# Performance work log

Hardware: AMD Instinct MI355X
Metric: run time of the kernel (lower is better)

## Reference

```python
import jax, jax.numpy as jnp
import numpy as np

FEAT_DIM = 256
NUM_HEADS = 8
HEAD_DIM = FEAT_DIM // NUM_HEADS
N_NODES = 4096
LN_EPS = 1e-5


def setup_inputs() -> dict:
    key = jax.random.key(0)
    ks = jax.random.split(key, 10)
    C = FEAT_DIM
    s = 1.0 / np.sqrt(C)
    x = jax.random.normal(ks[0], (N_NODES, C), dtype=jnp.float32)
    Wq = jax.random.uniform(ks[1], (C, C), jnp.float32, -s, s)
    bq = jax.random.uniform(ks[2], (C,), jnp.float32, -s, s)
    Wk = jax.random.uniform(ks[3], (C, C), jnp.float32, -s, s)
    bk = jax.random.uniform(ks[4], (C,), jnp.float32, -s, s)
    Wv = jax.random.uniform(ks[5], (C, C), jnp.float32, -s, s)
    bv = jax.random.uniform(ks[6], (C,), jnp.float32, -s, s)
    Wo = jax.random.uniform(ks[7], (C, C), jnp.float32, -s, s)
    bo = jax.random.uniform(ks[8], (C,), jnp.float32, -s, s)
    scale = jnp.float32(1.0 / np.sqrt(HEAD_DIM))
    gamma = jnp.ones((C,), jnp.float32)
    beta = jnp.zeros((C,), jnp.float32)
    return {"x": x, "Wq": Wq, "bq": bq, "Wk": Wk, "bk": bk, "Wv": Wv,
            "bv": bv, "scale": scale, "Wo": Wo, "bo": bo,
            "gamma": gamma, "beta": beta}


def reference(x, Wq, bq, Wk, bk, Wv, bv, scale, Wo, bo, gamma, beta):
    N, C = x.shape
    H, D = NUM_HEADS, HEAD_DIM
    q = (x @ Wq + bq).reshape(N, H, D)
    k = (x @ Wk + bk).reshape(N, H, D)
    v = (x @ Wv + bv).reshape(N, H, D)
    # scores[i, j, h]; softmax over j (the key/node axis), per original dim=1
    scores = jnp.einsum('ihd,jhd->ijh', q, k) * scale
    attn = jax.nn.softmax(scores, axis=1)
    messages = jnp.einsum('ijh,jhd->ihd', attn, v).reshape(N, H * D)
    y = x + messages @ Wo + bo
    # LayerNorm over last dim
    mu = jnp.mean(y, axis=-1, keepdims=True)
    var = jnp.mean(jnp.square(y - mu), axis=-1, keepdims=True)
    return (y - mu) * jax.lax.rsqrt(var + LN_EPS) * gamma + beta
```

## Files before the change

### kernel.cpp

```cpp
#include <hip/hip_runtime.h>
#include <hip/hip_bf16.h>
#include <math.h>

#define NN 4096
#define C  256
#define NH 8
#define HD 32
#define LN_EPS 1e-5f
#define LOG2E 1.44269504088896340736f

typedef unsigned short u16;
typedef __attribute__((ext_vector_type(8))) short bf16x8;
typedef __attribute__((ext_vector_type(4))) float f32x4;

__device__ inline u16 f2b(float f) {
    union { float f; unsigned u; } v; v.f = f;
    unsigned r = (v.u + 0x7fff + ((v.u >> 16) & 1)) >> 16;
    return (u16)r;
}

__device__ inline float fexp2(float x) {
#if __has_builtin(__builtin_amdgcn_exp2f)
    return __builtin_amdgcn_exp2f(x);
#else
    return exp2f(x);
#endif
}

__device__ inline unsigned pack_trunc(float e0, float e1) {
    return __builtin_amdgcn_perm(__float_as_uint(e1), __float_as_uint(e0),
                                 0x07060302u);
}

__device__ inline void atomic_add_agent(float* p, float v) {
    __hip_atomic_fetch_add(p, v, __ATOMIC_RELAXED, __HIP_MEMORY_SCOPE_AGENT);
}

__global__ __launch_bounds__(256) void prep_kernel(
    const float* __restrict__ Wq, const float* __restrict__ Wk,
    const float* __restrict__ Wv, const float* __restrict__ Wo,
    const float* __restrict__ x,
    u16* __restrict__ WqkvT, u16* __restrict__ WoT, u16* __restrict__ xb)
{
    const int z = blockIdx.z;
    if (z < 4) {
        __shared__ float tile[32][33];
        const float* W = (z == 0) ? Wq : (z == 1) ? Wk : (z == 2) ? Wv : Wo;
        u16* WT = (z == 3) ? WoT : (WqkvT + (size_t)z * 256 * 256);
        const int tx = threadIdx.x & 31, ty = threadIdx.x >> 5;
        const int n0 = blockIdx.x * 32, k0 = blockIdx.y * 32;
        #pragma unroll
        for (int i = 0; i < 32; i += 8)
            tile[ty + i][tx] = W[(size_t)(k0 + ty + i) * 256 + n0 + tx];
        __syncthreads();
        #pragma unroll
        for (int i = 0; i < 32; i += 8)
            WT[(size_t)(n0 + ty + i) * 256 + k0 + tx] = f2b(tile[tx][ty + i]);
    } else {
        const int slice = z - 4;
        const int bid = blockIdx.x * 8 + blockIdx.y;
        const int base = slice * (NN * C / 4) + bid * 4096 + threadIdx.x * 16;
        #pragma unroll
        for (int i = 0; i < 4; ++i) {
            const float4 v = *(const float4*)(x + base + i * 4);
            union { u16 u[4]; unsigned long long ull; } pk;
            pk.u[0] = f2b(v.x); pk.u[1] = f2b(v.y);
            pk.u[2] = f2b(v.z); pk.u[3] = f2b(v.w);
            *(unsigned long long*)(xb + base + i * 4) = pk.ull;
        }
    }
}

#define TRS 80
__global__ __launch_bounds__(256) void qkv_mfma_kernel(
    const u16* __restrict__ xb, const u16* __restrict__ WT,
    const float* __restrict__ bq, const float* __restrict__ bk,
    const float* __restrict__ bv, const float* __restrict__ scale_p,
    u16* __restrict__ qb, u16* __restrict__ kb, u16* __restrict__ vT)
{
    __shared__ u16 tr[64 * TRS];
    const int m0 = blockIdx.x * 64;
    const int n0 = blockIdx.y * 64;
    const int t = threadIdx.x;
    const int wave = t >> 6, lane = t & 63;
    const int l16 = lane & 15, quad = lane >> 4;

    f32x4 acc[4];
    #pragma unroll
    for (int ct = 0; ct < 4; ++ct) acc[ct] = f32x4{0.f, 0.f, 0.f, 0.f};

    const u16* xrow = xb + (size_t)(m0 + wave * 16 + l16) * C;
    #pragma unroll
    for (int kk = 0; kk < 8; ++kk) {
        const bf16x8 af = *(const bf16x8*)(xrow + kk * 32 + quad * 8);
        #pragma unroll
        for (int ct = 0; ct < 4; ++ct) {
            const bf16x8 bfr = *(const bf16x8*)(
                WT + (size_t)(n0 + ct * 16 + l16) * C + kk * 32 + quad * 8);
            acc[ct] = __builtin_amdgcn_mfma_f32_16x16x32_bf16(af, bfr, acc[ct], 0, 0, 0);
        }
    }

    const int sect = n0 >> 8;
    const int c0 = n0 & 255;
    const int rloc = wave * 16 + quad * 4;
    if (sect == 2) {
        #pragma unroll
        for (int ct = 0; ct < 4; ++ct) {
            const int c = c0 + ct * 16 + l16;
            const float b = bv[c];
            union { u16 u[4]; unsigned long long ull; } pk;
            #pragma unroll
            for (int r = 0; r < 4; ++r) pk.u[r] = f2b(acc[ct][r] + b);
            *(unsigned long long*)(vT + (size_t)c * NN + m0 + rloc) = pk.ull;
        }
    } else {
        const float scl = (sect == 0) ? (*scale_p) * LOG2E : 1.f;
        const float* bias = (sect == 0) ? bq : bk;
        #pragma unroll
        for (int ct = 0; ct < 4; ++ct) {
            const float b = bias[c0 + ct * 16 + l16];
            #pragma unroll
            for (int r = 0; r < 4; ++r)
                tr[(rloc + r) * TRS + ct * 16 + l16] = f2b((acc[ct][r] + b) * scl);
        }
        __syncthreads();
        const int row = t >> 2, chunk = t & 3;
        u16* dst = ((sect == 0) ? qb : kb)
                   + (size_t)(m0 + row) * C + c0 + chunk * 16;
        const u16* src = tr + row * TRS + chunk * 16;
        *(bf16x8*)(dst)     = *(const bf16x8*)(src);
        *(bf16x8*)(dst + 8) = *(const bf16x8*)(src + 8);
    }
}

#define TQ 64
#define TJ 64
#define NZ 4
#define ZT (NN / NZ)
#define KSTRIDE 40
#define VSTRIDE 72

__global__ __launch_bounds__(256) void attn_mfma_kernel(
    const u16* __restrict__ q, const u16* __restrict__ k,
    const u16* __restrict__ vT, float* __restrict__ msgacc,
    float* __restrict__ lacc)
{
    __shared__ u16 Ks[TJ * KSTRIDE];
    __shared__ u16 Vs[HD * VSTRIDE];
    __shared__ u16 Ps[4][16 * VSTRIDE];

    const int qbase = blockIdx.x * TQ;
    const int h = blockIdx.y;
    const int z = blockIdx.z;
    const int t = threadIdx.x;
    const int wave = t >> 6;
    const int lane = t & 63;
    const int l16 = lane & 15;
    const int quad = lane >> 4;

    const bf16x8 qfrag = *(const bf16x8*)(
        q + (size_t)(qbase + wave * 16 + l16) * C + h * HD + quad * 8);

    float lsum = 0.f;
    f32x4 o0 = {0.f, 0.f, 0.f, 0.f};
    f32x4 o1 = {0.f, 0.f, 0.f, 0.f};

    const int sj = t >> 2, sc = t & 3;
    const int sd = t >> 3, se = t & 7;

    for (int j0 = z * ZT; j0 < z * ZT + ZT; j0 += TJ) {
        __syncthreads();
        *(bf16x8*)(Ks + sj * KSTRIDE + sc * 8) =
            *(const bf16x8*)(k + (size_t)(j0 + sj) * C + h * HD + sc * 8);
        *(bf16x8*)(Vs + sd * VSTRIDE + se * 8) =
            *(const bf16x8*)(vT + (size_t)(h * HD + sd) * NN + j0 + se * 8);
        __syncthreads();

        f32x4 st[4];
        #pragma unroll
        for (int ct = 0; ct < 4; ++ct) {
            const bf16x8 kf = *(const bf16x8*)(Ks + (ct * 16 + l16) * KSTRIDE + quad * 8);
            f32x4 zz = {0.f, 0.f, 0.f, 0.f};
            st[ct] = __builtin_amdgcn_mfma_f32_16x16x32_bf16(kf, qfrag, zz, 0, 0, 0);
        }

        #pragma unroll
        for (int ct = 0; ct < 4; ++ct) {
            const float e0 = fexp2(st[ct][0]);
            const float e1 = fexp2(st[ct][1]);
            const float e2 = fexp2(st[ct][2]);
            const float e3 = fexp2(st[ct][3]);
            lsum += (e0 + e1) + (e2 + e3);
            const unsigned lo = pack_trunc(e0, e1);
            const unsigned hi = pack_trunc(e2, e3);
            *(unsigned long long*)(&Ps[wave][l16 * VSTRIDE + ct * 16 + quad * 4]) =
                (unsigned long long)lo | ((unsigned long long)hi << 32);
        }

        asm volatile("s_waitcnt lgkmcnt(0)" ::: "memory");

        #pragma unroll
        for (int ks = 0; ks < 2; ++ks) {
            const bf16x8 pf = *(const bf16x8*)(&Ps[wave][l16 * VSTRIDE + ks * 32 + quad * 8]);
            const bf16x8 vf0 = *(const bf16x8*)(Vs + l16 * VSTRIDE + ks * 32 + quad * 8);
            const bf16x8 vf1 = *(const bf16x8*)(Vs + (16 + l16) * VSTRIDE + ks * 32 + quad * 8);
            o0 = __builtin_amdgcn_mfma_f32_16x16x32_bf16(pf, vf0, o0, 0, 0, 0);
            o1 = __builtin_amdgcn_mfma_f32_16x16x32_bf16(pf, vf1, o1, 0, 0, 0);
        }
    }

    lsum += __shfl_xor(lsum, 16);
    lsum += __shfl_xor(lsum, 32);
    if (quad == 0)
        atomic_add_agent(&lacc[(size_t)(qbase + wave * 16 + l16) * NH + h], lsum);

    #pragma unroll
    for (int r = 0; r < 4; ++r) {
        const int row = qbase + wave * 16 + quad * 4 + r;
        atomic_add_agent(&msgacc[(size_t)row * C + h * HD + l16], o0[r]);
        atomic_add_agent(&msgacc[(size_t)row * C + h * HD + 16 + l16], o1[r]);
    }
}

#define OROWS 8
__global__ __launch_bounds__(256) void out_ln_mfma_kernel(
    const float* __restrict__ msgacc, const float* __restrict__ lacc,
    const u16* __restrict__ WoT, const float* __restrict__ bo,
    const float* __restrict__ x, const float* __restrict__ gamma,
    const float* __restrict__ beta, float* __restrict__ out)
{
    __shared__ float sums[2][4][OROWS];
    const int m0 = blockIdx.x * OROWS;
    const int t = threadIdx.x;
    const int w = t >> 6, lane = t & 63;
    const int l16 = lane & 15, quad = lane >> 4;

    f32x4 acc[4];
    #pragma unroll
    for (int ct = 0; ct < 4; ++ct) acc[ct] = f32x4{0.f, 0.f, 0.f, 0.f};

    const int ar = min(m0 + l16, NN - 1);
    const float* arow = msgacc + (size_t)ar * C;
    const float* lrow = lacc + (size_t)ar * NH;
    #pragma unroll
    for (int kk = 0; kk < 8; ++kk) {
        const float li = 1.f / lrow[kk];
        const float4 a0 = *(const float4*)(arow + kk * 32 + quad * 8);
        const float4 a1 = *(const float4*)(arow + kk * 32 + quad * 8 + 4);
        union { unsigned u[4]; bf16x8 v; } af;
        af.u[0] = pack_trunc(a0.x * li, a0.y * li);
        af.u[1] = pack_trunc(a0.z * li, a0.w * li);
        af.u[2] = pack_trunc(a1.x * li, a1.y * li);
        af.u[3] = pack_trunc(a1.z * li, a1.w * li);
        #pragma unroll
        for (int ct = 0; ct < 4; ++ct) {
            const bf16x8 bfr = *(const bf16x8*)(
                WoT + (size_t)(w * 64 + ct * 16 + l16) * C + kk * 32 + quad * 8);
            acc[ct] = __builtin_amdgcn_mfma_f32_16x16x32_bf16(af.v, bfr, acc[ct], 0, 0, 0);
        }
    }

    float val[4][4];
    if (quad < 2) {
        #pragma unroll
        for (int r = 0; r < 4; ++r) {
            const int row = m0 + quad * 4 + r;
            float sr = 0.f, qr = 0.f;
            #pragma unroll
            for (int ct = 0; ct < 4; ++ct) {
                const int c = w * 64 + ct * 16 + l16;
                const float v = acc[ct][r] + bo[c] + x[(size_t)row * C + c];
                val[ct][r] = v;
                sr += v;
                qr = fmaf(v, v, qr);
            }
            sr += __shfl_xor(sr, 1); sr += __shfl_xor(sr, 2);
            sr += __shfl_xor(sr, 4); sr += __shfl_xor(sr, 8);
            qr += __shfl_xor(qr, 1); qr += __shfl_xor(qr, 2);
            qr += __shfl_xor(qr, 4); qr += __shfl_xor(qr, 8);
            if (l16 == 0) {
                sums[0][w][quad * 4 + r] = sr;
                sums[1][w][quad * 4 + r] = qr;
            }
        }
    }
    __syncthreads();

    if (quad < 2) {
        #pragma unroll
        for (int r = 0; r < 4; ++r) {
            const int ri = quad * 4 + r;
            const int row = m0 + ri;
            const float tot  = sums[0][0][ri] + sums[0][1][ri] + sums[0][2][ri] + sums[0][3][ri];
            const float tot2 = sums[1][0][ri] + sums[1][1][ri] + sums[1][2][ri] + sums[1][3][ri];
            const float mu = tot * (1.f / C);
            const float var = fmaxf(tot2 * (1.f / C) - mu * mu, 0.f);
            const float rstd = rsqrtf(var + LN_EPS);
            #pragma unroll
            for (int ct = 0; ct < 4; ++ct) {
                const int c = w * 64 + ct * 16 + l16;
                out[(size_t)row * C + c] = (val[ct][r] - mu) * rstd * gamma[c] + beta[c];
            }
        }
    }
}

extern "C" void kernel_launch(void* const* d_in, const int* in_sizes, int n_in,
                              void* d_out, int out_size, void* d_ws, size_t ws_size,
                              hipStream_t stream) {
    const float* x     = (const float*)d_in[0];
    const float* Wq    = (const float*)d_in[1];
    const float* bq    = (const float*)d_in[2];
    const float* Wk    = (const float*)d_in[3];
    const float* bk    = (const float*)d_in[4];
    const float* Wv    = (const float*)d_in[5];
    const float* bv    = (const float*)d_in[6];
    const float* scale = (const float*)d_in[7];
    const float* Wo    = (const float*)d_in[8];
    const float* bo    = (const float*)d_in[9];
    const float* gamma = (const float*)d_in[10];
    const float* beta  = (const float*)d_in[11];
    float* out = (float*)d_out;

    u16* qb     = (u16*)d_ws;
    u16* kb     = qb + (size_t)NN * C;
    u16* vT     = kb + (size_t)NN * C;
    u16* xbuf   = vT + (size_t)NN * C;
    u16* WqkvT  = xbuf + (size_t)NN * C;
    u16* WoT    = WqkvT + (size_t)3 * C * C;
    float* msgacc = (float*)(WoT + (size_t)C * C);
    float* lacc   = msgacc + (size_t)NN * C;

    hipMemsetAsync(msgacc, 0, ((size_t)NN * C + (size_t)NN * NH) * sizeof(float),
                   stream);

    prep_kernel<<<dim3(8, 8, 8), 256, 0, stream>>>(Wq, Wk, Wv, Wo, x,
                                                   WqkvT, WoT, xbuf);
    qkv_mfma_kernel<<<dim3(NN / 64, 12), 256, 0, stream>>>(
        xbuf, WqkvT, bq, bk, bv, scale, qb, kb, vT);
    attn_mfma_kernel<<<dim3(NN / TQ, NH, NZ), 256, 0, stream>>>(
        qb, kb, vT, msgacc, lacc);
    out_ln_mfma_kernel<<<NN / OROWS, 256, 0, stream>>>(msgacc, lacc, WoT, bo, x,
                                                       gamma, beta, out);
}
```

Before: 158.0 us.

## Fuse all stages into one persistent cooperative kernel with grid syncs

```diff
diff --git a/kernel.cpp b/kernel.cpp
--- a/kernel.cpp
+++ b/kernel.cpp
@@ -1,6 +1,9 @@
 #include <hip/hip_runtime.h>
+#include <hip/hip_cooperative_groups.h>
 #include <hip/hip_bf16.h>
 #include <math.h>
+
+namespace cg = cooperative_groups;
 
 #define NN 4096
 #define C  256
@@ -13,6 +16,14 @@
 typedef __attribute__((ext_vector_type(8))) short bf16x8;
 typedef __attribute__((ext_vector_type(4))) float f32x4;
 
+#define TQ 64
+#define TJ 64
+#define KSTRIDE 40
+#define VSTRIDE 72
+#define TRS 80
+#define OROWS 8
+#define ZERO_FLOATS ((size_t)NN * C + (size_t)NN * NH)
+
 __device__ inline u16 f2b(float f) {
     union { float f; unsigned u; } v; v.f = f;
     unsigned r = (v.u + 0x7fff + ((v.u >> 16) & 1)) >> 16;
@@ -36,271 +47,281 @@
     __hip_atomic_fetch_add(p, v, __ATOMIC_RELAXED, __HIP_MEMORY_SCOPE_AGENT);
 }
 
-__global__ __launch_bounds__(256) void prep_kernel(
-    const float* __restrict__ Wq, const float* __restrict__ Wk,
-    const float* __restrict__ Wv, const float* __restrict__ Wo,
+struct SMemAttn {
+    u16 Ks[TJ * KSTRIDE];
+    u16 Vs[HD * VSTRIDE];
+    u16 Ps[4][16 * VSTRIDE];
+};
+union SMem {
+    SMemAttn a;
+    float tile[32][33];
+    u16 tr[64 * TRS];
+    float sums[2][4][OROWS];
+};
+
+__global__ __launch_bounds__(256, 6) void fused_kernel(
     const float* __restrict__ x,
-    u16* __restrict__ WqkvT, u16* __restrict__ WoT, u16* __restrict__ xb)
+    const float* __restrict__ Wq, const float* __restrict__ bq,
+    const float* __restrict__ Wk, const float* __restrict__ bk,
+    const float* __restrict__ Wv, const float* __restrict__ bv,
+    const float* __restrict__ scale_p,
+    const float* __restrict__ Wo, const float* __restrict__ bo,
+    const float* __restrict__ gamma, const float* __restrict__ beta,
+    float* __restrict__ out,
+    u16* __restrict__ qb, u16* __restrict__ kb, u16* __restrict__ vT,
+    u16* __restrict__ xbuf, u16* __restrict__ WqkvT, u16* __restrict__ WoT,
+    float* __restrict__ msgacc, float* __restrict__ lacc, int NZC)
 {
-    const int z = blockIdx.z;
-    if (z < 4) {
-        __shared__ float tile[32][33];
-        const float* W = (z == 0) ? Wq : (z == 1) ? Wk : (z == 2) ? Wv : Wo;
-        u16* WT = (z == 3) ? WoT : (WqkvT + (size_t)z * 256 * 256);
-        const int tx = threadIdx.x & 31, ty = threadIdx.x >> 5;
-        const int n0 = blockIdx.x * 32, k0 = blockIdx.y * 32;
-        #pragma unroll
-        for (int i = 0; i < 32; i += 8)
-            tile[ty + i][tx] = W[(size_t)(k0 + ty + i) * 256 + n0 + tx];
-        __syncthreads();
-        #pragma unroll
-        for (int i = 0; i < 32; i += 8)
-            WT[(size_t)(n0 + ty + i) * 256 + k0 + tx] = f2b(tile[tx][ty + i]);
-    } else {
-        const int slice = z - 4;
-        const int bid = blockIdx.x * 8 + blockIdx.y;
-        const int base = slice * (NN * C / 4) + bid * 4096 + threadIdx.x * 16;
-        #pragma unroll
-        for (int i = 0; i < 4; ++i) {
-            const float4 v = *(const float4*)(x + base + i * 4);
-            union { u16 u[4]; unsigned long long ull; } pk;
-            pk.u[0] = f2b(v.x); pk.u[1] = f2b(v.y);
-            pk.u[2] = f2b(v.z); pk.u[3] = f2b(v.w);
-            *(unsigned long long*)(xb + base + i * 4) = pk.ull;
-        }
-    }
-}
-
-#define TRS 80
-__global__ __launch_bounds__(256) void qkv_mfma_kernel(
-    const u16* __restrict__ xb, const u16* __restrict__ WT,
-    const float* __restrict__ bq, const float* __restrict__ bk,
-    const float* __restrict__ bv, const float* __restrict__ scale_p,
-    u16* __restrict__ qb, u16* __restrict__ kb, u16* __restrict__ vT)
-{
-    __shared__ u16 tr[64 * TRS];
-    const int m0 = blockIdx.x * 64;
-    const int n0 = blockIdx.y * 64;
+    __shared__ SMem sm;
+    cg::grid_group grid = cg::this_grid();
+    const int G = gridDim.x;
     const int t = threadIdx.x;
     const int wave = t >> 6, lane = t & 63;
     const int l16 = lane & 15, quad = lane >> 4;
 
-    f32x4 acc[4];
-    #pragma unroll
-    for (int ct = 0; ct < 4; ++ct) acc[ct] = f32x4{0.f, 0.f, 0.f, 0.f};
-
-    const u16* xrow = xb + (size_t)(m0 + wave * 16 + l16) * C;
-    #pragma unroll
-    for (int kk = 0; kk < 8; ++kk) {
-        const bf16x8 af = *(const bf16x8*)(xrow + kk * 32 + quad * 8);
-        #pragma unroll
-        for (int ct = 0; ct < 4; ++ct) {
-            const bf16x8 bfr = *(const bf16x8*)(
-                WT + (size_t)(n0 + ct * 16 + l16) * C + kk * 32 + quad * 8);
-            acc[ct] = __builtin_amdgcn_mfma_f32_16x16x32_bf16(af, bfr, acc[ct], 0, 0, 0);
-        }
-    }
-
-    const int sect = n0 >> 8;
-    const int c0 = n0 & 255;
-    const int rloc = wave * 16 + quad * 4;
-    if (sect == 2) {
-        #pragma unroll
-        for (int ct = 0; ct < 4; ++ct) {
-            const int c = c0 + ct * 16 + l16;
-            const float b = bv[c];
-            union { u16 u[4]; unsigned long long ull; } pk;
-            #pragma unroll
-            for (int r = 0; r < 4; ++r) pk.u[r] = f2b(acc[ct][r] + b);
-            *(unsigned long long*)(vT + (size_t)c * NN + m0 + rloc) = pk.ull;
-        }
-    } else {
-        const float scl = (sect == 0) ? (*scale_p) * LOG2E : 1.f;
-        const float* bias = (sect == 0) ? bq : bk;
-        #pragma unroll
-        for (int ct = 0; ct < 4; ++ct) {
-            const float b = bias[c0 + ct * 16 + l16];
-            #pragma unroll
-            for (int r = 0; r < 4; ++r)
-                tr[(rloc + r) * TRS + ct * 16 + l16] = f2b((acc[ct][r] + b) * scl);
-        }
+    {
+        const size_t start = ((size_t)blockIdx.x * 256 + t) * 4;
+        const size_t step = (size_t)G * 1024;
+        const float4 zf = {0.f, 0.f, 0.f, 0.f};
+        for (size_t i = start; i < ZERO_FLOATS; i += step)
+            *(float4*)(msgacc + i) = zf;
+    }
+    for (int job = blockIdx.x; job < 512; job += G) {
+        if (job < 256) {
+            const int z = job >> 6;
+            const int sub = job & 63;
+            const int n0 = (sub & 7) * 32, k0 = (sub >> 3) * 32;
+            const float* W = (z == 0) ? Wq : (z == 1) ? Wk : (z == 2) ? Wv : Wo;
+            u16* WT = (z == 3) ? WoT : (WqkvT + (size_t)z * 65536);
+            const int tx = t & 31, ty = t >> 5;
+            __syncthreads();
+            #pragma unroll
+            for (int i = 0; i < 32; i += 8)
+                sm.tile[ty + i][tx] = W[(size_t)(k0 + ty + i) * 256 + n0 + tx];
+            __syncthreads();
+            #pragma unroll
+            for (int i = 0; i < 32; i += 8)
+                WT[(size_t)(n0 + ty + i) * 256 + k0 + tx] = f2b(sm.tile[tx][ty + i]);
+        } else {
+            const int base = (job - 256) * 4096 + t * 16;
+            #pragma unroll
+            for (int i = 0; i < 4; ++i) {
+                const float4 v = *(const float4*)(x + base + i * 4);
+                union { u16 u[4]; unsigned long long ull; } pk;
+                pk.u[0] = f2b(v.x); pk.u[1] = f2b(v.y);
+                pk.u[2] = f2b(v.z); pk.u[3] = f2b(v.w);
+                *(unsigned long long*)(xbuf + base + i * 4) = pk.ull;
+            }
+        }
+    }
+    grid.sync();
+
+    for (int job = blockIdx.x; job < 768; job += G) {
+        const int m0 = (job & 63) * 64;
+        const int n0 = (job >> 6) * 64;
+
+        f32x4 acc[4];
+        #pragma unroll
+        for (int ct = 0; ct < 4; ++ct) acc[ct] = f32x4{0.f, 0.f, 0.f, 0.f};
+
+        const u16* xrow = xbuf + (size_t)(m0 + wave * 16 + l16) * C;
+        #pragma unroll
+        for (int kk = 0; kk < 8; ++kk) {
+            const bf16x8 af = *(const bf16x8*)(xrow + kk * 32 + quad * 8);
+            #pragma unroll
+            for (int ct = 0; ct < 4; ++ct) {
+                const bf16x8 bfr = *(const bf16x8*)(
+                    WqkvT + (size_t)(n0 + ct * 16 + l16) * C + kk * 32 + quad * 8);
+                acc[ct] = __builtin_amdgcn_mfma_f32_16x16x32_bf16(af, bfr, acc[ct], 0, 0, 0);
+            }
+        }
+
+        const int sect = n0 >> 8;
+        const int c0 = n0 & 255;
+        const int rloc = wave * 16 + quad * 4;
+        if (sect == 2) {
+            #pragma unroll
+            for (int ct = 0; ct < 4; ++ct) {
+                const int c = c0 + ct * 16 + l16;
+                const float b = bv[c];
+                union { u16 u[4]; unsigned long long ull; } pk;
+                #pragma unroll
+                for (int r = 0; r < 4; ++r) pk.u[r] = f2b(acc[ct][r] + b);
+                *(unsigned long long*)(vT + (size_t)c * NN + m0 + rloc) = pk.ull;
+            }
+        } else {
+            const float scl = (sect == 0) ? (*scale_p) * LOG2E : 1.f;
+            const float* bias = (sect == 0) ? bq : bk;
+            __syncthreads();
+            #pragma unroll
+            for (int ct = 0; ct < 4; ++ct) {
+                const float b = bias[c0 + ct * 16 + l16];
+                #pragma unroll
+                for (int r = 0; r < 4; ++r)
+                    sm.tr[(rloc + r) * TRS + ct * 16 + l16] =
+                        f2b((acc[ct][r] + b) * scl);
+            }
+            __syncthreads();
+            const int row = t >> 2, chunk = t & 3;
+            u16* dst = ((sect == 0) ? qb : kb)
+                       + (size_t)(m0 + row) * C + c0 + chunk * 16;
+            const u16* src = sm.tr + row * TRS + chunk * 16;
+            *(bf16x8*)(dst)     = *(const bf16x8*)(src);
+            *(bf16x8*)(dst + 8) = *(const bf16x8*)(src + 8);
+        }
+    }
+    grid.sync();
+
+    for (int job = blockIdx.x; job < 512 * NZC; job += G) {
+        const int qbase = (job & 63) * TQ;
+        const int h = (job >> 6) & 7;
+        const int z = job >> 9;
+        const int tile0 = (64 * z) / NZC, tile1 = (64 * (z + 1)) / NZC;
+
+        const bf16x8 qfrag = *(const bf16x8*)(
+            qb + (size_t)(qbase + wave * 16 + l16) * C + h * HD + quad * 8);
+
+        float lsum = 0.f;
+        f32x4 o0 = {0.f, 0.f, 0.f, 0.f};
+        f32x4 o1 = {0.f, 0.f, 0.f, 0.f};
+
+        const int sj = t >> 2, sc = t & 3;
+        const int sd = t >> 3, se = t & 7;
+
+        for (int j0 = tile0 * TJ; j0 < tile1 * TJ; j0 += TJ) {
+            __syncthreads();
+            *(bf16x8*)(sm.a.Ks + sj * KSTRIDE + sc * 8) =
+                *(const bf16x8*)(kb + (size_t)(j0 + sj) * C + h * HD + sc * 8);
+            *(bf16x8*)(sm.a.Vs + sd * VSTRIDE + se * 8) =
+                *(const bf16x8*)(vT + (size_t)(h * HD + sd) * NN + j0 + se * 8);
+            __syncthreads();
+
+            f32x4 st[4];
+            #pragma unroll
+            for (int ct = 0; ct < 4; ++ct) {
+                const bf16x8 kf = *(const bf16x8*)(
+                    sm.a.Ks + (ct * 16 + l16) * KSTRIDE + quad * 8);
+                f32x4 zz = {0.f, 0.f, 0.f, 0.f};
+                st[ct] = __builtin_amdgcn_mfma_f32_16x16x32_bf16(kf, qfrag, zz, 0, 0, 0);
+            }
+
+            #pragma unroll
+            for (int ct = 0; ct < 4; ++ct) {
+                const float e0 = fexp2(st[ct][0]);
+                const float e1 = fexp2(st[ct][1]);
+                const float e2 = fexp2(st[ct][2]);
+                const float e3 = fexp2(st[ct][3]);
+                lsum += (e0 + e1) + (e2 + e3);
+                const unsigned lo = pack_trunc(e0, e1);
+                const unsigned hi = pack_trunc(e2, e3);
+                *(unsigned long long*)(
+                    &sm.a.Ps[wave][l16 * VSTRIDE + ct * 16 + quad * 4]) =
+                    (unsigned long long)lo | ((unsigned long long)hi << 32);
+            }
+
+            asm volatile("s_waitcnt lgkmcnt(0)" ::: "memory");
+
+            #pragma unroll
+            for (int ks = 0; ks < 2; ++ks) {
+                const bf16x8 pf = *(const bf16x8*)(
+                    &sm.a.Ps[wave][l16 * VSTRIDE + ks * 32 + quad * 8]);
+                const bf16x8 vf0 = *(const bf16x8*)(
+                    sm.a.Vs + l16 * VSTRIDE + ks * 32 + quad * 8);
+                const bf16x8 vf1 = *(const bf16x8*)(
+                    sm.a.Vs + (16 + l16) * VSTRIDE + ks * 32 + quad * 8);
+                o0 = __builtin_amdgcn_mfma_f32_16x16x32_bf16(pf, vf0, o0, 0, 0, 0);
+                o1 = __builtin_amdgcn_mfma_f32_16x16x32_bf16(pf, vf1, o1, 0, 0, 0);
+            }
+        }
+
+        lsum += __shfl_xor(lsum, 16);
+        lsum += __shfl_xor(lsum, 32);
+        if (quad == 0)
+            atomic_add_agent(&lacc[(size_t)(qbase + wave * 16 + l16) * NH + h], lsum);
+
+        #pragma unroll
+        for (int r = 0; r < 4; ++r) {
+            const int row = qbase + wave * 16 + quad * 4 + r;
+            atomic_add_agent(&msgacc[(size_t)row * C + h * HD + l16], o0[r]);
+            atomic_add_agent(&msgacc[(size_t)row * C + h * HD + 16 + l16], o1[r]);
+        }
+    }
+    grid.sync();
+
+    for (int job = blockIdx.x; job < NN / OROWS; job += G) {
+        const int m0 = job * OROWS;
+        const int w = wave;
+
+        f32x4 acc[4];
+        #pragma unroll
+        for (int ct = 0; ct < 4; ++ct) acc[ct] = f32x4{0.f, 0.f, 0.f, 0.f};
+
+        const int ar = min(m0 + l16, NN - 1);
+        const float* arow = msgacc + (size_t)ar * C;
+        const float* lrow = lacc + (size_t)ar * NH;
+        #pragma unroll
+        for (int kk = 0; kk < 8; ++kk) {
+            const float li = 1.f / lrow[kk];
+            const float4 a0 = *(const float4*)(arow + kk * 32 + quad * 8);
+            const float4 a1 = *(const float4*)(arow + kk * 32 + quad * 8 + 4);
+            union { unsigned u[4]; bf16x8 v; } af;
+            af.u[0] = pack_trunc(a0.x * li, a0.y * li);
+            af.u[1] = pack_trunc(a0.z * li, a0.w * li);
+            af.u[2] = pack_trunc(a1.x * li, a1.y * li);
+            af.u[3] = pack_trunc(a1.z * li, a1.w * li);
+            #pragma unroll
+            for (int ct = 0; ct < 4; ++ct) {
+                const bf16x8 bfr = *(const bf16x8*)(
+                    WoT + (size_t)(w * 64 + ct * 16 + l16) * C + kk * 32 + quad * 8);
+                acc[ct] = __builtin_amdgcn_mfma_f32_16x16x32_bf16(af.v, bfr, acc[ct], 0, 0, 0);
+            }
+        }
+
         __syncthreads();
-        const int row = t >> 2, chunk = t & 3;
-        u16* dst = ((sect == 0) ? qb : kb)
-                   + (size_t)(m0 + row) * C + c0 + chunk * 16;
-        const u16* src = tr + row * TRS + chunk * 16;
-        *(bf16x8*)(dst)     = *(const bf16x8*)(src);
-        *(bf16x8*)(dst + 8) = *(const bf16x8*)(src + 8);
-    }
-}
-
-#define TQ 64
-#define TJ 64
-#define NZ 4
-#define ZT (NN / NZ)
-#define KSTRIDE 40
-#define VSTRIDE 72
-
-__global__ __launch_bounds__(256) void attn_mfma_kernel(
-    const u16* __restrict__ q, const u16* __restrict__ k,
-    const u16* __restrict__ vT, float* __restrict__ msgacc,
-    float* __restrict__ lacc)
-{
-    __shared__ u16 Ks[TJ * KSTRIDE];
-    __shared__ u16 Vs[HD * VSTRIDE];
-    __shared__ u16 Ps[4][16 * VSTRIDE];
-
-    const int qbase = blockIdx.x * TQ;
-    const int h = blockIdx.y;
-    const int z = blockIdx.z;
-    const int t = threadIdx.x;
-    const int wave = t >> 6;
-    const int lane = t & 63;
-    const int l16 = lane & 15;
-    const int quad = lane >> 4;
-
-    const bf16x8 qfrag = *(const bf16x8*)(
-        q + (size_t)(qbase + wave * 16 + l16) * C + h * HD + quad * 8);
-
-    float lsum = 0.f;
-    f32x4 o0 = {0.f, 0.f, 0.f, 0.f};
-    f32x4 o1 = {0.f, 0.f, 0.f, 0.f};
-
-    const int sj = t >> 2, sc = t & 3;
-    const int sd = t >> 3, se = t & 7;
-
-    for (int j0 = z * ZT; j0 < z * ZT + ZT; j0 += TJ) {
+        float val[4][4];
+        if (quad < 2) {
+            #pragma unroll
+            for (int r = 0; r < 4; ++r) {
+                const int row = m0 + quad * 4 + r;
+                float sr = 0.f, qr = 0.f;
+                #pragma unroll
+                for (int ct = 0; ct < 4; ++ct) {
+                    const int c = w * 64 + ct * 16 + l16;
+                    const float v = acc[ct][r] + bo[c] + x[(size_t)row * C + c];
+                    val[ct][r] = v;
+                    sr += v;
+                    qr = fmaf(v, v, qr);
+                }
+                sr += __shfl_xor(sr, 1); sr += __shfl_xor(sr, 2);
+                sr += __shfl_xor(sr, 4); sr += __shfl_xor(sr, 8);
+                qr += __shfl_xor(qr, 1); qr += __shfl_xor(qr, 2);
+                qr += __shfl_xor(qr, 4); qr += __shfl_xor(qr, 8);
+                if (l16 == 0) {
+                    sm.sums[0][w][quad * 4 + r] = sr;
+                    sm.sums[1][w][quad * 4 + r] = qr;
+                }
+            }
+        }
         __syncthreads();
-        *(bf16x8*)(Ks + sj * KSTRIDE + sc * 8) =
-            *(const bf16x8*)(k + (size_t)(j0 + sj) * C + h * HD + sc * 8);
-        *(bf16x8*)(Vs + sd * VSTRIDE + se * 8) =
-            *(const bf16x8*)(vT + (size_t)(h * HD + sd) * NN + j0 + se * 8);
-        __syncthreads();
-
-        f32x4 st[4];
-        #pragma unroll
-        for (int ct = 0; ct < 4; ++ct) {
-            const bf16x8 kf = *(const bf16x8*)(Ks + (ct * 16 + l16) * KSTRIDE + quad * 8);
-            f32x4 zz = {0.f, 0.f, 0.f, 0.f};
-            st[ct] = __builtin_amdgcn_mfma_f32_16x16x32_bf16(kf, qfrag, zz, 0, 0, 0);
-        }
-
-        #pragma unroll
-        for (int ct = 0; ct < 4; ++ct) {
-            const float e0 = fexp2(st[ct][0]);
-            const float e1 = fexp2(st[ct][1]);
-            const float e2 = fexp2(st[ct][2]);
-            const float e3 = fexp2(st[ct][3]);
-            lsum += (e0 + e1) + (e2 + e3);
-            const unsigned lo = pack_trunc(e0, e1);
-            const unsigned hi = pack_trunc(e2, e3);
-            *(unsigned long long*)(&Ps[wave][l16 * VSTRIDE + ct * 16 + quad * 4]) =
-                (unsigned long long)lo | ((unsigned long long)hi << 32);
-        }
-
-        asm volatile("s_waitcnt lgkmcnt(0)" ::: "memory");
-
-        #pragma unroll
-        for (int ks = 0; ks < 2; ++ks) {
-            const bf16x8 pf = *(const bf16x8*)(&Ps[wave][l16 * VSTRIDE + ks * 32 + quad * 8]);
-            const bf16x8 vf0 = *(const bf16x8*)(Vs + l16 * VSTRIDE + ks * 32 + quad * 8);
-            const bf16x8 vf1 = *(const bf16x8*)(Vs + (16 + l16) * VSTRIDE + ks * 32 + quad * 8);
-            o0 = __builtin_amdgcn_mfma_f32_16x16x32_bf16(pf, vf0, o0, 0, 0, 0);
-            o1 = __builtin_amdgcn_mfma_f32_16x16x32_bf16(pf, vf1, o1, 0, 0, 0);
-        }
-    }
-
-    lsum += __shfl_xor(lsum, 16);
-    lsum += __shfl_xor(lsum, 32);
-    if (quad == 0)
-        atomic_add_agent(&lacc[(size_t)(qbase + wave * 16 + l16) * NH + h], lsum);
-
-    #pragma unroll
-    for (int r = 0; r < 4; ++r) {
-        const int row = qbase + wave * 16 + quad * 4 + r;
-        atomic_add_agent(&msgacc[(size_t)row * C + h * HD + l16], o0[r]);
-        atomic_add_agent(&msgacc[(size_t)row * C + h * HD + 16 + l16], o1[r]);
-    }
-}
-
-#define OROWS 8
-__global__ __launch_bounds__(256) void out_ln_mfma_kernel(
-    const float* __restrict__ msgacc, const float* __restrict__ lacc,
-    const u16* __restrict__ WoT, const float* __restrict__ bo,
-    const float* __restrict__ x, const float* __restrict__ gamma,
-    const float* __restrict__ beta, float* __restrict__ out)
-{
-    __shared__ float sums[2][4][OROWS];
-    const int m0 = blockIdx.x * OROWS;
-    const int t = threadIdx.x;
-    const int w = t >> 6, lane = t & 63;
-    const int l16 = lane & 15, quad = lane >> 4;
-
-    f32x4 acc[4];
-    #pragma unroll
-    for (int ct = 0; ct < 4; ++ct) acc[ct] = f32x4{0.f, 0.f, 0.f, 0.f};
-
-    const int ar = min(m0 + l16, NN - 1);
-    const float* arow = msgacc + (size_t)ar * C;
-    const float* lrow = lacc + (size_t)ar * NH;
-    #pragma unroll
-    for (int kk = 0; kk < 8; ++kk) {
-        const float li = 1.f / lrow[kk];
-        const float4 a0 = *(const float4*)(arow + kk * 32 + quad * 8);
-        const float4 a1 = *(const float4*)(arow + kk * 32 + quad * 8 + 4);
-        union { unsigned u[4]; bf16x8 v; } af;
-        af.u[0] = pack_trunc(a0.x * li, a0.y * li);
-        af.u[1] = pack_trunc(a0.z * li, a0.w * li);
-        af.u[2] = pack_trunc(a1.x * li, a1.y * li);
-        af.u[3] = pack_trunc(a1.z * li, a1.w * li);
-        #pragma unroll
-        for (int ct = 0; ct < 4; ++ct) {
-            const bf16x8 bfr = *(const bf16x8*)(
-                WoT + (size_t)(w * 64 + ct * 16 + l16) * C + kk * 32 + quad * 8);
-            acc[ct] = __builtin_amdgcn_mfma_f32_16x16x32_bf16(af.v, bfr, acc[ct], 0, 0, 0);
-        }
-    }
-
-    float val[4][4];
-    if (quad < 2) {
-        #pragma unroll
-        for (int r = 0; r < 4; ++r) {
-            const int row = m0 + quad * 4 + r;
-            float sr = 0.f, qr = 0.f;
-            #pragma unroll
-            for (int ct = 0; ct < 4; ++ct) {
-                const int c = w * 64 + ct * 16 + l16;
-                const float v = acc[ct][r] + bo[c] + x[(size_t)row * C + c];
-                val[ct][r] = v;
-                sr += v;
-                qr = fmaf(v, v, qr);
-            }
-            sr += __shfl_xor(sr, 1); sr += __shfl_xor(sr, 2);
-            sr += __shfl_xor(sr, 4); sr += __shfl_xor(sr, 8);
-            qr += __shfl_xor(qr, 1); qr += __shfl_xor(qr, 2);
-            qr += __shfl_xor(qr, 4); qr += __shfl_xor(qr, 8);
-            if (l16 == 0) {
-                sums[0][w][quad * 4 + r] = sr;
-                sums[1][w][quad * 4 + r] = qr;
-            }
-        }
-    }
-    __syncthreads();
-
-    if (quad < 2) {
-        #pragma unroll
-        for (int r = 0; r < 4; ++r) {
-            const int ri = quad * 4 + r;
-            const int row = m0 + ri;
-            const float tot  = sums[0][0][ri] + sums[0][1][ri] + sums[0][2][ri] + sums[0][3][ri];
-            const float tot2 = sums[1][0][ri] + sums[1][1][ri] + sums[1][2][ri] + sums[1][3][ri];
-            const float mu = tot * (1.f / C);
-            const float var = fmaxf(tot2 * (1.f / C) - mu * mu, 0.f);
-            const float rstd = rsqrtf(var + LN_EPS);
-            #pragma unroll
-            for (int ct = 0; ct < 4; ++ct) {
-                const int c = w * 64 + ct * 16 + l16;
-                out[(size_t)row * C + c] = (val[ct][r] - mu) * rstd * gamma[c] + beta[c];
+
+        if (quad < 2) {
+            #pragma unroll
+            for (int r = 0; r < 4; ++r) {
+                const int ri = quad * 4 + r;
+                const int row = m0 + ri;
+                const float tot  = sm.sums[0][0][ri] + sm.sums[0][1][ri]
+                                 + sm.sums[0][2][ri] + sm.sums[0][3][ri];
+                const float tot2 = sm.sums[1][0][ri] + sm.sums[1][1][ri]
+                                 + sm.sums[1][2][ri] + sm.sums[1][3][ri];
+                const float mu = tot * (1.f / C);
+                const float var = fmaxf(tot2 * (1.f / C) - mu * mu, 0.f);
+                const float rstd = rsqrtf(var + LN_EPS);
+                #pragma unroll
+                for (int ct = 0; ct < 4; ++ct) {
+                    const int c = w * 64 + ct * 16 + l16;
+                    out[(size_t)row * C + c] =
+                        (val[ct][r] - mu) * rstd * gamma[c] + beta[c];
+                }
             }
         }
     }
@@ -332,15 +353,20 @@
     float* msgacc = (float*)(WoT + (size_t)C * C);
     float* lacc   = msgacc + (size_t)NN * C;
 
-    hipMemsetAsync(msgacc, 0, ((size_t)NN * C + (size_t)NN * NH) * sizeof(float),
-                   stream);
-
-    prep_kernel<<<dim3(8, 8, 8), 256, 0, stream>>>(Wq, Wk, Wv, Wo, x,
-                                                   WqkvT, WoT, xbuf);
-    qkv_mfma_kernel<<<dim3(NN / 64, 12), 256, 0, stream>>>(
-        xbuf, WqkvT, bq, bk, bv, scale, qb, kb, vT);
-    attn_mfma_kernel<<<dim3(NN / TQ, NH, NZ), 256, 0, stream>>>(
-        qb, kb, vT, msgacc, lacc);
-    out_ln_mfma_kernel<<<NN / OROWS, 256, 0, stream>>>(msgacc, lacc, WoT, bo, x,
-                                                       gamma, beta, out);
-}
+    int maxB = 0;
+    hipOccupancyMaxActiveBlocksPerMultiprocessor(&maxB, fused_kernel, 256, 0);
+    if (maxB < 1) maxB = 1;
+    int G = maxB * 256;
+    if (G > 2048) G = 2048;
+    if (G >= 512) G = (G / 512) * 512;
+    int NZC = (G >= 512) ? (G / 512) : 1;
+
+    void* args[] = {
+        (void*)&x, (void*)&Wq, (void*)&bq, (void*)&Wk, (void*)&bk,
+        (void*)&Wv, (void*)&bv, (void*)&scale, (void*)&Wo, (void*)&bo,
+        (void*)&gamma, (void*)&beta, (void*)&out,
+        (void*)&qb, (void*)&kb, (void*)&vT, (void*)&xbuf,
+        (void*)&WqkvT, (void*)&WoT, (void*)&msgacc, (void*)&lacc, (void*)&NZC,
+    };
+    hipLaunchCooperativeKernel(fused_kernel, dim3(G), dim3(256), args, 0, stream);
+}
```

After: 425.3 us. 2.69x slower.
